# Kernel optimization log

Hardware: AMD Instinct MI355X
Metric: run time of the kernel (lower is better)

## Reference

```python
import jax, jax.numpy as jnp
import numpy as np

N_NODES = 100000
N_EDGES = 600000
D = 128
C = 16


def setup_inputs() -> dict:
    key = jax.random.key(0)
    k1, k2, k3, k4, k5 = jax.random.split(key, 5)
    h = jax.random.normal(k1, (N_NODES, D), dtype=jnp.float32)
    edge_src = jax.random.randint(k2, (N_EDGES,), 0, N_NODES, dtype=jnp.int32)
    edge_dst = jax.random.randint(k3, (N_EDGES,), 0, N_NODES, dtype=jnp.int32)
    W = jax.random.normal(k4, (C, 2 * D), dtype=jnp.float32) * (1.0 / np.sqrt(2 * D))
    b = jax.random.normal(k5, (C,), dtype=jnp.float32) * 0.01
    return {"h": h, "edge_src": edge_src, "edge_dst": edge_dst, "W": W, "b": b}


def reference(h, edge_src, edge_dst, W, b):
    # Gather per-edge src/dst node features: [E, D] each
    h_src = h[edge_src]
    h_dst = h[edge_dst]
    # Split W into src/dst halves to avoid materializing the [E, 2D] concat
    W_src = W[:, :D]  # [C, D]
    W_dst = W[:, D:]  # [C, D]
    # score = cat([h_src, h_dst], -1) @ W.T + b, computed as two GEMMs
    score = jnp.einsum('ed,cd->ec', h_src, W_src) \
          + jnp.einsum('ed,cd->ec', h_dst, W_dst) + b
    return score  # [E, C]
```

## Files before the change

### kernel.cpp

```cpp
#include <hip/hip_runtime.h>
#include <hip/hip_bf16.h>

#define DIMS 128
#define NCLS 16
#define NPROJ 32

typedef __attribute__((ext_vector_type(8))) short bf16x8;
typedef __attribute__((ext_vector_type(4))) float f32x4;

__device__ inline short f2bf(float f) {
  unsigned u = __builtin_bit_cast(unsigned, f);
  u += 0x7fffu + ((u >> 16) & 1u);
  return (short)(u >> 16);
}

__device__ inline bf16x8 pack8(float4 a, float4 b) {
  bf16x8 r;
  r[0] = f2bf(a.x); r[1] = f2bf(a.y); r[2] = f2bf(a.z); r[3] = f2bf(a.w);
  r[4] = f2bf(b.x); r[5] = f2bf(b.y); r[6] = f2bf(b.z); r[7] = f2bf(b.w);
  return r;
}

__global__ __launch_bounds__(256) void proj_mfma_kernel(
    const float* __restrict__ h, const float* __restrict__ W,
    const float* __restrict__ b, float* __restrict__ P, int n_nodes) {
  const int lane = threadIdx.x & 63;
  const int wave = threadIdx.x >> 6;
  const int row_base = blockIdx.x * 64 + wave * 16;
  if (row_base >= n_nodes) return;

  const int m  = lane & 15;
  const int kg = lane >> 4;

  int row = row_base + m;
  int row_c = row < n_nodes ? row : n_nodes - 1;

  const float* hrow = h + (size_t)row_c * DIMS;
  bf16x8 afrag[4];
#pragma unroll
  for (int ks = 0; ks < 4; ++ks) {
    float4 f0 = *reinterpret_cast<const float4*>(hrow + ks * 32 + kg * 8);
    float4 f1 = *reinterpret_cast<const float4*>(hrow + ks * 32 + kg * 8 + 4);
    afrag[ks] = pack8(f0, f1);
  }

  const float* wrow = W + (size_t)m * (2 * DIMS);
  bf16x8 bfrag[2][4];
#pragma unroll
  for (int half = 0; half < 2; ++half) {
#pragma unroll
    for (int ks = 0; ks < 4; ++ks) {
      const float* wp = wrow + half * DIMS + ks * 32 + kg * 8;
      float4 f0 = *reinterpret_cast<const float4*>(wp);
      float4 f1 = *reinterpret_cast<const float4*>(wp + 4);
      bfrag[half][ks] = pack8(f0, f1);
    }
  }

  f32x4 acc0 = {0.f, 0.f, 0.f, 0.f};
  f32x4 acc1 = {0.f, 0.f, 0.f, 0.f};
#pragma unroll
  for (int ks = 0; ks < 4; ++ks) {
    acc0 = __builtin_amdgcn_mfma_f32_16x16x32_bf16(afrag[ks], bfrag[0][ks], acc0, 0, 0, 0);
    acc1 = __builtin_amdgcn_mfma_f32_16x16x32_bf16(afrag[ks], bfrag[1][ks], acc1, 0, 0, 0);
  }

  float bias = b[m];
#pragma unroll
  for (int r = 0; r < 4; ++r) {
    int orow = row_base + kg * 4 + r;
    if (orow < n_nodes) {
      P[(size_t)orow * NPROJ + m]        = acc0[r] + bias;
      P[(size_t)orow * NPROJ + NCLS + m] = acc1[r];
    }
  }
}

__global__ __launch_bounds__(256) void gather_kernel(
    const int* __restrict__ esrc, const int* __restrict__ edst,
    const float* __restrict__ P, float* __restrict__ out, int n_edges) {
  long t = (long)blockIdx.x * blockDim.x + threadIdx.x;
  int e = (int)(t >> 4);
  if (e >= n_edges) return;
  int c = (int)(t & 15);
  int s = esrc[e];
  int d = edst[e];
  float v = P[(size_t)s * NPROJ + c] + P[(size_t)d * NPROJ + NCLS + c];
  __builtin_nontemporal_store(v, &out[t]);
}

__global__ __launch_bounds__(256) void direct_kernel(
    const float* __restrict__ h, const int* __restrict__ esrc,
    const int* __restrict__ edst, const float* __restrict__ W,
    const float* __restrict__ b, float* __restrict__ out, int n_edges) {
  long t = (long)blockIdx.x * blockDim.x + threadIdx.x;
  int e = (int)(t >> 4);
  if (e >= n_edges) return;
  int c = (int)(t & 15);
  const float* hs = h + (size_t)esrc[e] * DIMS;
  const float* hd = h + (size_t)edst[e] * DIMS;
  float acc = b[c];
  for (int d0 = 0; d0 < DIMS; ++d0) {
    acc = fmaf(hs[d0], W[c * 2 * DIMS + d0], acc);
    acc = fmaf(hd[d0], W[c * 2 * DIMS + DIMS + d0], acc);
  }
  out[t] = acc;
}

extern "C" void kernel_launch(void* const* d_in, const int* in_sizes, int n_in,
                              void* d_out, int out_size, void* d_ws, size_t ws_size,
                              hipStream_t stream) {
  const float* h    = (const float*)d_in[0];
  const int*   esrc = (const int*)d_in[1];
  const int*   edst = (const int*)d_in[2];
  const float* W    = (const float*)d_in[3];
  const float* b    = (const float*)d_in[4];
  float* out = (float*)d_out;

  int n_nodes = in_sizes[0] / DIMS;
  int n_edges = in_sizes[1];

  size_t need = (size_t)n_nodes * NPROJ * sizeof(float);
  if (ws_size >= need) {
    float* P = (float*)d_ws;
    int blocks1 = (n_nodes + 63) / 64;
    proj_mfma_kernel<<<blocks1, 256, 0, stream>>>(h, W, b, P, n_nodes);
    long total = (long)n_edges * NCLS;
    int blocks2 = (int)((total + 255) / 256);
    gather_kernel<<<blocks2, 256, 0, stream>>>(esrc, edst, P, out, n_edges);
  } else {
    long total = (long)n_edges * NCLS;
    int blocks2 = (int)((total + 255) / 256);
    direct_kernel<<<blocks2, 256, 0, stream>>>(h, esrc, edst, W, b, out, n_edges);
  }
}
```

Measured before the change: 135.7 us.

## Store node projections as split bf16 planes and gather eight classes per thread

```diff
diff --git a/kernel.cpp b/kernel.cpp
--- a/kernel.cpp
+++ b/kernel.cpp
@@ -14,6 +14,11 @@
   return (short)(u >> 16);
 }
 
+__device__ inline float bf2f(unsigned short u) {
+  unsigned x = ((unsigned)u) << 16;
+  return __builtin_bit_cast(float, x);
+}
+
 __device__ inline bf16x8 pack8(float4 a, float4 b) {
   bf16x8 r;
   r[0] = f2bf(a.x); r[1] = f2bf(a.y); r[2] = f2bf(a.z); r[3] = f2bf(a.w);
@@ -23,7 +28,8 @@
 
 __global__ __launch_bounds__(256) void proj_mfma_kernel(
     const float* __restrict__ h, const float* __restrict__ W,
-    const float* __restrict__ b, float* __restrict__ P, int n_nodes) {
+    const float* __restrict__ b, unsigned short* __restrict__ Psrc,
+    unsigned short* __restrict__ Pdst, int n_nodes) {
   const int lane = threadIdx.x & 63;
   const int wave = threadIdx.x >> 6;
   const int row_base = blockIdx.x * 64 + wave * 16;
@@ -70,23 +76,33 @@
   for (int r = 0; r < 4; ++r) {
     int orow = row_base + kg * 4 + r;
     if (orow < n_nodes) {
-      P[(size_t)orow * NPROJ + m]        = acc0[r] + bias;
-      P[(size_t)orow * NPROJ + NCLS + m] = acc1[r];
+      Psrc[(size_t)orow * NCLS + m] = (unsigned short)f2bf(acc0[r] + bias);
+      Pdst[(size_t)orow * NCLS + m] = (unsigned short)f2bf(acc1[r]);
     }
   }
 }
 
-__global__ __launch_bounds__(256) void gather_kernel(
+__global__ __launch_bounds__(256) void gather2_kernel(
     const int* __restrict__ esrc, const int* __restrict__ edst,
-    const float* __restrict__ P, float* __restrict__ out, int n_edges) {
+    const unsigned short* __restrict__ Psrc, const unsigned short* __restrict__ Pdst,
+    float* __restrict__ out, int n_edges) {
   long t = (long)blockIdx.x * blockDim.x + threadIdx.x;
-  int e = (int)(t >> 4);
+  int e = (int)(t >> 1);
   if (e >= n_edges) return;
-  int c = (int)(t & 15);
+  int q = (int)(t & 1);
   int s = esrc[e];
   int d = edst[e];
-  float v = P[(size_t)s * NPROJ + c] + P[(size_t)d * NPROJ + NCLS + c];
-  __builtin_nontemporal_store(v, &out[t]);
+  bf16x8 vs = *reinterpret_cast<const bf16x8*>(Psrc + (size_t)s * NCLS + q * 8);
+  bf16x8 vd = *reinterpret_cast<const bf16x8*>(Pdst + (size_t)d * NCLS + q * 8);
+  f32x4 lo, hi;
+#pragma unroll
+  for (int j = 0; j < 4; ++j) {
+    lo[j] = bf2f((unsigned short)vs[j]) + bf2f((unsigned short)vd[j]);
+    hi[j] = bf2f((unsigned short)vs[j + 4]) + bf2f((unsigned short)vd[j + 4]);
+  }
+  float* op = out + (size_t)t * 8;
+  __builtin_nontemporal_store(lo, reinterpret_cast<f32x4*>(op));
+  __builtin_nontemporal_store(hi, reinterpret_cast<f32x4*>(op + 4));
 }
 
 __global__ __launch_bounds__(256) void direct_kernel(
@@ -120,14 +136,16 @@
   int n_nodes = in_sizes[0] / DIMS;
   int n_edges = in_sizes[1];
 
-  size_t need = (size_t)n_nodes * NPROJ * sizeof(float);
+  size_t plane = (size_t)n_nodes * NCLS * sizeof(unsigned short);
+  size_t need = 2 * ((plane + 255) & ~(size_t)255);
   if (ws_size >= need) {
-    float* P = (float*)d_ws;
+    unsigned short* Psrc = (unsigned short*)d_ws;
+    unsigned short* Pdst = (unsigned short*)((char*)d_ws + ((plane + 255) & ~(size_t)255));
     int blocks1 = (n_nodes + 63) / 64;
-    proj_mfma_kernel<<<blocks1, 256, 0, stream>>>(h, W, b, P, n_nodes);
-    long total = (long)n_edges * NCLS;
+    proj_mfma_kernel<<<blocks1, 256, 0, stream>>>(h, W, b, Psrc, Pdst, n_nodes);
+    long total = (long)n_edges * 2;
     int blocks2 = (int)((total + 255) / 256);
-    gather_kernel<<<blocks2, 256, 0, stream>>>(esrc, edst, P, out, n_edges);
+    gather2_kernel<<<blocks2, 256, 0, stream>>>(esrc, edst, Psrc, Pdst, out, n_edges);
   } else {
     long total = (long)n_edges * NCLS;
     int blocks2 = (int)((total + 255) / 256);
```

Result: faster. 128.6 us (-5.2%).
